# Kernel optimization log

Hardware: AMD Instinct MI355X
Metric: run time of the kernel (lower is better)

## Reference

```python
import jax, jax.numpy as jnp
import numpy as np
import math

B, S_IMG, S_TXT = 1, 2048, 256
D_MODEL, HEADS, HEAD_DIM = 3072, 24, 128
INNER = HEADS * HEAD_DIM
EPS = 1e-6


def _rmsnorm(x, scale):
    # flax-style RMSNorm over last dim, fp32 stats
    x32 = x.astype(jnp.float32)
    var = jnp.mean(x32 * x32, axis=-1, keepdims=True)
    return ((x32 * jax.lax.rsqrt(var + EPS)).astype(x.dtype)) * scale


def _rope(x, cos, sin):
    # x: [B,S,H,D]; cos,sin: [S,D]; interleaved-pair rotation (use_real_unbind_dim=-1)
    c = cos[None, :, None, :].astype(jnp.float32)
    s = sin[None, :, None, :].astype(jnp.float32)
    xp = x.reshape(*x.shape[:-1], -1, 2)
    x_rot = jnp.stack([-xp[..., 1], xp[..., 0]], axis=-1).reshape(x.shape)
    return (x.astype(jnp.float32) * c + x_rot.astype(jnp.float32) * s).astype(x.dtype)


def setup_inputs() -> dict:
    key = jax.random.key(0)
    ks = jax.random.split(key, 16)
    w = lambda k, shp: jax.random.normal(k, shp, jnp.float32) * 0.02
    S = S_TXT + S_IMG
    pos = jnp.arange(S, dtype=jnp.float32)
    inv_freq = 1.0 / (10000.0 ** (jnp.arange(0, HEAD_DIM, 2, dtype=jnp.float32) / HEAD_DIM))
    ang = pos[:, None] * inv_freq[None, :]  # [S, D/2]
    cos = jnp.repeat(jnp.cos(ang), 2, axis=-1)  # [S, D] paired layout
    sin = jnp.repeat(jnp.sin(ang), 2, axis=-1)
    return {
        'hidden_states': jax.random.normal(ks[0], (B, S_IMG, D_MODEL), jnp.float32),
        'encoder_hidden_states': jax.random.normal(ks[1], (B, S_TXT, D_MODEL), jnp.float32),
        'cos': cos,
        'sin': sin,
        'wq': w(ks[2], (D_MODEL, INNER)),
        'wk': w(ks[3], (D_MODEL, INNER)),
        'wv': w(ks[4], (D_MODEL, INNER)),
        'wq_add': w(ks[5], (D_MODEL, INNER)),
        'wk_add': w(ks[6], (D_MODEL, INNER)),
        'wv_add': w(ks[7], (D_MODEL, INNER)),
        'bq_add': w(ks[8], (INNER,)),
        'bk_add': w(ks[9], (INNER,)),
        'bv_add': w(ks[10], (INNER,)),
        'norm_q': jnp.ones((HEAD_DIM,), jnp.float32),
        'norm_k': jnp.ones((HEAD_DIM,), jnp.float32),
        'norm_add_q': jnp.ones((HEAD_DIM,), jnp.float32),
        'norm_add_k': jnp.ones((HEAD_DIM,), jnp.float32),
        'w_out': w(ks[11], (INNER, D_MODEL)),
        'b_out': w(ks[12], (D_MODEL,)),
        'w_add_out': w(ks[13], (INNER, D_MODEL)),
        'b_add_out': w(ks[14], (D_MODEL,)),
    }


def reference(hidden_states, encoder_hidden_states, cos, sin, wq, wk, wv,
              wq_add, wk_add, wv_add, bq_add, bk_add, bv_add,
              norm_q, norm_k, norm_add_q, norm_add_k,
              w_out, b_out, w_add_out, b_add_out):
    St = encoder_hidden_states.shape[1]
    heads = lambda x: x.reshape(x.shape[0], x.shape[1], HEADS, HEAD_DIM)
    # image-token q/k/v + QK RMSNorm
    q = _rmsnorm(heads(hidden_states @ wq), norm_q)
    k = _rmsnorm(heads(hidden_states @ wk), norm_k)
    v = heads(hidden_states @ wv)
    # encoder-token q/k/v (biased projections) + QK RMSNorm
    eq = _rmsnorm(heads(encoder_hidden_states @ wq_add + bq_add), norm_add_q)
    ek = _rmsnorm(heads(encoder_hidden_states @ wk_add + bk_add), norm_add_k)
    ev = heads(encoder_hidden_states @ wv_add + bv_add)
    # encoder tokens concatenated first
    q = jnp.concatenate([eq, q], axis=1)
    k = jnp.concatenate([ek, k], axis=1)
    v = jnp.concatenate([ev, v], axis=1)
    q = _rope(q, cos, sin)
    k = _rope(k, cos, sin)
    # naive softmax attention
    scale = 1.0 / math.sqrt(HEAD_DIM)
    attn = jnp.einsum('bshd,bthd->bhst', q, k) * scale
    attn = jax.nn.softmax(attn, axis=-1)
    out = jnp.einsum('bhst,bthd->bshd', attn, v)
    out = out.reshape(out.shape[0], out.shape[1], -1)
    # split back into encoder / image streams and apply output projections
    enc_out = out[:, :St] @ w_add_out + b_add_out
    img_out = out[:, St:] @ w_out + b_out
    return (img_out, enc_out)
```

## Files before the change

### kernel.cpp

```cpp
#include <hip/hip_runtime.h>
#include <hip/hip_bf16.h>

typedef unsigned short u16;
typedef unsigned int   u32;
typedef __bf16 bf16x8 __attribute__((ext_vector_type(8)));
typedef float  f32x4  __attribute__((ext_vector_type(4)));

#define SEQ   2304
#define DM    3072
#define NH    24
#define HD    128
#define S_TXT 256
#define S_IMG 2048
#define SCALE 0.08838834764831845f

__device__ __forceinline__ u16 f2bf(float x) {
  u32 u = __float_as_uint(x);
  u += 0x7fffu + ((u >> 16) & 1u);
  return (u16)(u >> 16);
}
__device__ __forceinline__ float bf2f(u16 b) {
  return __uint_as_float(((u32)b) << 16);
}
__device__ __forceinline__ f32x4 zero4() { f32x4 z = {0.f, 0.f, 0.f, 0.f}; return z; }
__device__ __forceinline__ u32 cvtpk(float lo, float hi) {
  u32 r;
  asm("v_cvt_pk_bf16_f32 %0, %1, %2" : "=v"(r) : "v"(lo), "v"(hi));
  return r;
}

#define GLDS16(gp, lp) __builtin_amdgcn_global_load_lds( \
    (__attribute__((address_space(1))) void*)(gp),       \
    (__attribute__((address_space(3))) void*)(lp), 16, 0, 0)

__global__ __launch_bounds__(256) void conv_bf16_k(const float* __restrict__ src,
                                                   u16* __restrict__ dst, int n4) {
  int i = blockIdx.x * 256 + threadIdx.x;
  if (i >= n4) return;
  float4 v = ((const float4*)src)[i];
  ushort4 o;
  o.x = f2bf(v.x); o.y = f2bf(v.y); o.z = f2bf(v.z); o.w = f2bf(v.w);
  ((ushort4*)dst)[i] = o;
}

struct WP { const float* s[8]; u16* d[8]; };

__global__ __launch_bounds__(256) void w_transpose_k(WP p) {
  __shared__ float tile[32][33];
  const float* __restrict__ src = p.s[blockIdx.z];
  u16* __restrict__ dst = p.d[blockIdx.z];
  const int c0 = blockIdx.x * 32, r0 = blockIdx.y * 32;
  const int tx = threadIdx.x & 31, ty = threadIdx.x >> 5;
#pragma unroll
  for (int i = 0; i < 4; ++i)
    tile[ty + i*8][tx] = src[(size_t)(r0 + ty + i*8) * DM + c0 + tx];
  __syncthreads();
#pragma unroll
  for (int i = 0; i < 4; ++i)
    dst[(size_t)(c0 + ty + i*8) * DM + r0 + tx] = f2bf(tile[tx][ty + i*8]);
}

__global__ __launch_bounds__(256) void v_transpose_k(const u16* __restrict__ V,
                                                     u16* __restrict__ Vt) {
  __shared__ u16 tile[32][34];
  const int h = blockIdx.z;
  const int t0 = blockIdx.x * 32, d0 = blockIdx.y * 32;
  const int tx = threadIdx.x & 31, ty = threadIdx.x >> 5;
#pragma unroll
  for (int i = 0; i < 4; ++i)
    tile[ty + i*8][tx] = V[((size_t)h * SEQ + t0 + ty + i*8) * HD + d0 + tx];
  __syncthreads();
#pragma unroll
  for (int i = 0; i < 4; ++i)
    Vt[((size_t)h * HD + d0 + ty + i*8) * SEQ + t0 + tx] = tile[tx][ty + i*8];
}

__global__ __launch_bounds__(256) void gemm_bt_k(
    const u16* __restrict__ A,
    const u16* __restrict__ B0, const u16* __restrict__ B1, const u16* __restrict__ B2,
    const float* __restrict__ bias0, const float* __restrict__ bias1, const float* __restrict__ bias2,
    void* __restrict__ out0, void* __restrict__ out1, void* __restrict__ out2,
    int row_off, int mode) {
  __shared__ __attribute__((aligned(128))) char As[128*128];
  __shared__ __attribute__((aligned(128))) char Bs[128*128];
  const int bz = blockIdx.z;
  const u16* __restrict__ Bm = (bz == 0) ? B0 : ((bz == 1) ? B1 : B2);
  const float* __restrict__ bias = (bz == 0) ? bias0 : ((bz == 1) ? bias1 : bias2);
  void* out = (bz == 0) ? out0 : ((bz == 1) ? out1 : out2);
  const int bm = blockIdx.x, bn = blockIdx.y;
  const int tid = threadIdx.x;
  const int w = tid >> 6, l = tid & 63;
  const int wr = w >> 1, wc = w & 1;

  f32x4 acc[4][4];
#pragma unroll
  for (int mi = 0; mi < 4; ++mi)
#pragma unroll
    for (int ni = 0; ni < 4; ++ni) acc[mi][ni] = zero4();

  const int srow  = l >> 3;
  const int scolb = ((l & 7) ^ srow) << 4;
  const char* Ag = (const char*)(A  + (size_t)(bm*128 + w*32) * DM) + (size_t)srow * (DM*2) + scolb;
  const char* Bg = (const char*)(Bm + (size_t)(bn*128 + w*32) * DM) + (size_t)srow * (DM*2) + scolb;
  char* AsW = As + (w*32) * 128;
  char* BsW = Bs + (w*32) * 128;

  for (int kt = 0; kt < DM/64; ++kt) {
#pragma unroll
    for (int i = 0; i < 4; ++i) {
      GLDS16(Ag + (size_t)i*8*(DM*2) + kt*128, AsW + i*8*128);
      GLDS16(Bg + (size_t)i*8*(DM*2) + kt*128, BsW + i*8*128);
    }
    __syncthreads();
#pragma unroll
    for (int kk = 0; kk < 2; ++kk) {
      bf16x8 af[4], bfr[4];
#pragma unroll
      for (int mi = 0; mi < 4; ++mi) {
        const int row = wr*64 + mi*16 + (l & 15);
        const int cb  = ((kk << 6) + ((l >> 4) << 4)) ^ ((row & 7) << 4);
        af[mi] = *(const bf16x8*)(As + row*128 + cb);
      }
#pragma unroll
      for (int ni = 0; ni < 4; ++ni) {
        const int row = wc*64 + ni*16 + (l & 15);
        const int cb  = ((kk << 6) + ((l >> 4) << 4)) ^ ((row & 7) << 4);
        bfr[ni] = *(const bf16x8*)(Bs + row*128 + cb);
      }
#pragma unroll
      for (int mi = 0; mi < 4; ++mi)
#pragma unroll
        for (int ni = 0; ni < 4; ++ni)
          acc[mi][ni] = __builtin_amdgcn_mfma_f32_16x16x32_bf16(af[mi], bfr[ni], acc[mi][ni], 0, 0, 0);
    }
    __syncthreads();
  }

#pragma unroll
  for (int mi = 0; mi < 4; ++mi) {
    const int mbase = bm*128 + wr*64 + mi*16 + ((l >> 4) << 2);
#pragma unroll
    for (int ni = 0; ni < 4; ++ni) {
      const int ncol = bn*128 + wc*64 + ni*16 + (l & 15);
      const float bv = bias ? bias[ncol] : 0.f;
#pragma unroll
      for (int r = 0; r < 4; ++r) {
        const float v = acc[mi][ni][r] + bv;
        if (mode == 0) {
          ((u16*)out)[((size_t)bn * SEQ + (row_off + mbase + r)) * HD + (ncol & 127)] = f2bf(v);
        } else {
          ((float*)out)[(size_t)(mbase + r) * DM + ncol] = v;
        }
      }
    }
  }
}

__global__ __launch_bounds__(256) void qk_norm_rope_k(
    const u16* __restrict__ Qf, const u16* __restrict__ Kf,
    u16* __restrict__ Qb, u16* __restrict__ Kb,
    const float* __restrict__ cosT, const float* __restrict__ sinT,
    const float* __restrict__ nq, const float* __restrict__ nk,
    const float* __restrict__ naq, const float* __restrict__ nak) {
  const int gw = (blockIdx.x * 256 + threadIdx.x) >> 6;
  const int l = threadIdx.x & 63;
  const int which = (gw >= NH * SEQ) ? 1 : 0;
  const int rem = which ? (gw - NH * SEQ) : gw;
  const int h = rem / SEQ, t = rem % SEQ;
  const size_t base = ((size_t)h * SEQ + t) * HD + l * 2;
  const ushort2 xb = *(const ushort2*)((which ? Kf : Qf) + base);
  const float x0 = bf2f(xb.x), x1 = bf2f(xb.y);
  float ss = x0*x0 + x1*x1;
#pragma unroll
  for (int msk = 1; msk < 64; msk <<= 1) ss += __shfl_xor(ss, msk, 64);
  const float rr = rsqrtf(ss * (1.0f/128.0f) + 1e-6f);
  const float* nw = which ? (t < S_TXT ? nak : nk) : (t < S_TXT ? naq : nq);
  const float n0 = x0 * rr * nw[l*2], n1 = x1 * rr * nw[l*2 + 1];
  const float c = cosT[(size_t)t * HD + l*2], sn = sinT[(size_t)t * HD + l*2];
  float o0 = n0 * c - n1 * sn;
  float o1 = n1 * c + n0 * sn;
  if (!which) { o0 *= SCALE; o1 *= SCALE; }
  ushort2 ob; ob.x = f2bf(o0); ob.y = f2bf(o1);
  *(ushort2*)((which ? Kb : Qb) + base) = ob;
}

__global__ __launch_bounds__(256) void attn_k(
    const u16* __restrict__ Q, const u16* __restrict__ K,
    const u16* __restrict__ Vt, u16* __restrict__ O) {
  __shared__ __attribute__((aligned(128))) char Kl[64*256];
  __shared__ __attribute__((aligned(128))) char Vl[128*128];
  __shared__ __attribute__((aligned(128))) char Pl[4][2][2048];
  const int qb = blockIdx.x, h = blockIdx.y;
  const int tid = threadIdx.x, w = tid >> 6, l = tid & 63;
  const int g = l >> 4, q16 = l & 15;

  const u16* Qh = Q  + ((size_t)h * SEQ + qb*128 + w*32) * HD;
  const u16* Kh = K  + (size_t)h * SEQ * HD;
  const u16* Vh = Vt + (size_t)h * HD * SEQ;

  bf16x8 qf[2][4];
#pragma unroll
  for (int qt = 0; qt < 2; ++qt)
#pragma unroll
    for (int kf = 0; kf < 4; ++kf)
      qf[qt][kf] = *(const bf16x8*)(Qh + (qt*16 + q16) * HD + kf*32 + g*8);

  f32x4 o[2][8];
#pragma unroll
  for (int qt = 0; qt < 2; ++qt)
#pragma unroll
    for (int db = 0; db < 8; ++db) o[qt][db] = zero4();
  float m[2]  = {-3e38f, -3e38f};
  float rl[2] = {0.f, 0.f};

  const int vswz = ((l & 7) ^ (l >> 3)) << 4;
  const int pswz = (q16 & 7) << 4;

  for (int kb = 0; kb < SEQ/64; ++kb) {
#pragma unroll
    for (int i = 0; i < 4; ++i) {
      const int rloc = i*4 + (l >> 4);
      const int colb = ((l & 15) << 4) ^ ((rloc & 7) << 4);
      GLDS16((const char*)Kh + ((size_t)(kb*64 + w*16 + rloc)) * 256 + colb,
             Kl + (w*16 + i*4) * 256);
    }
#pragma unroll
    for (int i = 0; i < 4; ++i) {
      const int rloc = w*32 + i*8 + (l >> 3);
      GLDS16((const char*)Vh + (size_t)rloc * (SEQ*2) + kb*128 + vswz,
             Vl + (w*32 + i*8) * 128);
    }
    __syncthreads();

    f32x4 s[2][4];
#pragma unroll
    for (int qt = 0; qt < 2; ++qt)
#pragma unroll
      for (int mi = 0; mi < 4; ++mi) s[qt][mi] = zero4();
#pragma unroll
    for (int mi = 0; mi < 4; ++mi) {
      const int row = mi*16 + q16;
      bf16x8 kfr[4];
#pragma unroll
      for (int kf = 0; kf < 4; ++kf) {
        const int cb = ((kf << 6) + (g << 4)) ^ ((row & 7) << 4);
        kfr[kf] = *(const bf16x8*)(Kl + row*256 + cb);
      }
#pragma unroll
      for (int kf = 0; kf < 4; ++kf) {
        s[0][mi] = __builtin_amdgcn_mfma_f32_16x16x32_bf16(kfr[kf], qf[0][kf], s[0][mi], 0, 0, 0);
        s[1][mi] = __builtin_amdgcn_mfma_f32_16x16x32_bf16(kfr[kf], qf[1][kf], s[1][mi], 0, 0, 0);
      }
    }

    float rsv[2];
#pragma unroll
    for (int qt = 0; qt < 2; ++qt) {
      float mx = s[qt][0][0];
#pragma unroll
      for (int mi = 0; mi < 4; ++mi)
#pragma unroll
        for (int r = 0; r < 4; ++r) mx = fmaxf(mx, s[qt][mi][r]);
      mx = fmaxf(mx, __shfl_xor(mx, 16, 64));
      mx = fmaxf(mx, __shfl_xor(mx, 32, 64));
      const float mn = fmaxf(m[qt], mx);
      rsv[qt] = __expf(m[qt] - mn);
      m[qt] = mn;
      float sum = 0.f;
#pragma unroll
      for (int mi = 0; mi < 4; ++mi) {
        f32x4 t = s[qt][mi];
#pragma unroll
        for (int r = 0; r < 4; ++r) { t[r] = __expf(t[r] - mn); sum += t[r]; }
        s[qt][mi] = t;
      }
      sum += __shfl_xor(sum, 16, 64);
      sum += __shfl_xor(sum, 32, 64);
      rl[qt] = rl[qt] * rsv[qt] + sum;
      char* Pw = Pl[w][qt];
#pragma unroll
      for (int mi = 0; mi < 4; ++mi) {
        uint2 pk;
        pk.x = cvtpk(s[qt][mi][0], s[qt][mi][1]);
        pk.y = cvtpk(s[qt][mi][2], s[qt][mi][3]);
        *(uint2*)(Pw + ((q16*128 + mi*32 + g*8) ^ pswz)) = pk;
      }
    }

#pragma unroll
    for (int qt = 0; qt < 2; ++qt) {
      float rs4[4];
#pragma unroll
      for (int r = 0; r < 4; ++r)
        rs4[r] = __shfl(rsv[qt], (g << 4) + (g << 2) + r, 64);
#pragma unroll
      for (int db = 0; db < 8; ++db) {
        f32x4 t = o[qt][db];
#pragma unroll
        for (int r = 0; r < 4; ++r) t[r] *= rs4[r];
        o[qt][db] = t;
      }
    }

    bf16x8 pa[2][2];
#pragma unroll
    for (int qt = 0; qt < 2; ++qt)
#pragma unroll
      for (int kblk = 0; kblk < 2; ++kblk)
        pa[qt][kblk] = *(const bf16x8*)(Pl[w][qt] + ((q16*128 + kblk*64 + g*16) ^ pswz));

#pragma unroll
    for (int kblk = 0; kblk < 2; ++kblk)
#pragma unroll
      for (int db = 0; db < 8; ++db) {
        const int vrow = db*16 + q16;
        const int vcb  = ((kblk << 6) + (g << 4)) ^ ((vrow & 7) << 4);
        bf16x8 vb = *(const bf16x8*)(Vl + vrow*128 + vcb);
        o[0][db] = __builtin_amdgcn_mfma_f32_16x16x32_bf16(pa[0][kblk], vb, o[0][db], 0, 0, 0);
        o[1][db] = __builtin_amdgcn_mfma_f32_16x16x32_bf16(pa[1][kblk], vb, o[1][db], 0, 0, 0);
      }
    __syncthreads();
  }

#pragma unroll
  for (int qt = 0; qt < 2; ++qt) {
    float inv4[4];
#pragma unroll
    for (int r = 0; r < 4; ++r)
      inv4[r] = 1.f / __shfl(rl[qt], (g << 4) + (g << 2) + r, 64);
#pragma unroll
    for (int db = 0; db < 8; ++db)
#pragma unroll
      for (int r = 0; r < 4; ++r) {
        const int token = qb*128 + w*32 + qt*16 + g*4 + r;
        const int col = h*HD + db*16 + q16;
        O[(size_t)token * DM + col] = f2bf(o[qt][db][r] * inv4[r]);
      }
  }
}

extern "C" void kernel_launch(void* const* d_in, const int* in_sizes, int n_in,
                              void* d_out, int out_size, void* d_ws, size_t ws_size,
                              hipStream_t stream) {
  const float* hidden = (const float*)d_in[0];
  const float* ench   = (const float*)d_in[1];
  const float* cosT   = (const float*)d_in[2];
  const float* sinT   = (const float*)d_in[3];
  const float* wq  = (const float*)d_in[4];
  const float* wk  = (const float*)d_in[5];
  const float* wv  = (const float*)d_in[6];
  const float* wqa = (const float*)d_in[7];
  const float* wka = (const float*)d_in[8];
  const float* wva = (const float*)d_in[9];
  const float* bqa = (const float*)d_in[10];
  const float* bka = (const float*)d_in[11];
  const float* bva = (const float*)d_in[12];
  const float* nq  = (const float*)d_in[13];
  const float* nk  = (const float*)d_in[14];
  const float* naq = (const float*)d_in[15];
  const float* nak = (const float*)d_in[16];
  const float* w_out     = (const float*)d_in[17];
  const float* b_out     = (const float*)d_in[18];
  const float* w_add_out = (const float*)d_in[19];
  const float* b_add_out = (const float*)d_in[20];
  float* outp = (float*)d_out;
  (void)in_sizes; (void)n_in; (void)out_size; (void)ws_size;

  char* ws = (char*)d_ws;
  size_t off = 0;
  auto alloc = [&](size_t n) { char* p = ws + off; off += (n + 255) & ~(size_t)255; return p; };
  u16* wt[8];
  for (int i = 0; i < 8; ++i) wt[i] = (u16*)alloc((size_t)DM * DM * 2);
  u16* xb_img = (u16*)alloc((size_t)S_IMG * DM * 2);
  u16* xb_enc = (u16*)alloc((size_t)S_TXT * DM * 2);
  u16* Qf = (u16*)alloc((size_t)NH * SEQ * HD * 2);
  u16* Kf = (u16*)alloc((size_t)NH * SEQ * HD * 2);
  u16* Vf = (u16*)alloc((size_t)NH * SEQ * HD * 2);
  u16* Qb = (u16*)alloc((size_t)NH * SEQ * HD * 2);
  u16* Kb = (u16*)alloc((size_t)NH * SEQ * HD * 2);
  u16* Vt = (u16*)alloc((size_t)NH * HD * SEQ * 2);
  u16* Ob = (u16*)alloc((size_t)SEQ * DM * 2);

  conv_bf16_k<<<(S_IMG*DM/4)/256, 256, 0, stream>>>(hidden, xb_img, S_IMG*DM/4);
  conv_bf16_k<<<(S_TXT*DM/4)/256, 256, 0, stream>>>(ench, xb_enc, S_TXT*DM/4);

  WP wp;
  wp.s[0] = wq;  wp.s[1] = wk;  wp.s[2] = wv;
  wp.s[3] = wqa; wp.s[4] = wka; wp.s[5] = wva;
  wp.s[6] = w_out; wp.s[7] = w_add_out;
  for (int i = 0; i < 8; ++i) wp.d[i] = wt[i];
  w_transpose_k<<<dim3(96, 96, 8), 256, 0, stream>>>(wp);

  gemm_bt_k<<<dim3(16, 24, 3), 256, 0, stream>>>(xb_img, wt[0], wt[1], wt[2],
      nullptr, nullptr, nullptr, Qf, Kf, Vf, S_TXT, 0);
  gemm_bt_k<<<dim3(2, 24, 3), 256, 0, stream>>>(xb_enc, wt[3], wt[4], wt[5],
      bqa, bka, bva, Qf, Kf, Vf, 0, 0);

  qk_norm_rope_k<<<(2*NH*SEQ)/4, 256, 0, stream>>>(Qf, Kf, Qb, Kb, cosT, sinT, nq, nk, naq, nak);
  v_transpose_k<<<dim3(SEQ/32, HD/32, NH), 256, 0, stream>>>(Vf, Vt);

  attn_k<<<dim3(SEQ/128, NH), 256, 0, stream>>>(Qb, Kb, Vt, Ob);

  gemm_bt_k<<<dim3(16, 24, 1), 256, 0, stream>>>(Ob + (size_t)S_TXT * DM, wt[6], wt[6], wt[6],
      b_out, b_out, b_out, outp, outp, outp, 0, 1);
  gemm_bt_k<<<dim3(2, 24, 1), 256, 0, stream>>>(Ob, wt[7], wt[7], wt[7],
      b_add_out, b_add_out, b_add_out,
      outp + (size_t)S_IMG * DM, outp + (size_t)S_IMG * DM, outp + (size_t)S_IMG * DM, 0, 1);
}
```

Measured before the change: 937.8 us.

## Double-buffer attention K/V tiles, remap attention blocks, merge enc/img GEMM launches

The attention kernel now double-buffers its K and V shared-memory tiles, prefetching the next tile while computing the current one. It replaces __syncthreads with explicit waitcnt and barrier calls and raises wave priority around the MFMA sections. The attention grid is flattened and remapped so blocks are spread across XCDs by head. The separate encoder and image QKV and output-projection GEMMs are merged into single launches over a concatenated activation buffer, choosing weights and bias per row block. This removes kernel launches and tail effects, at the cost of more LDS use per attention block, which may reduce occupancy.

```diff
diff --git a/kernel.cpp b/kernel.cpp
--- a/kernel.cpp
+++ b/kernel.cpp
@@ -75,19 +75,28 @@
     Vt[((size_t)h * HD + d0 + ty + i*8) * SEQ + t0 + tx] = tile[tx][ty + i*8];
 }
 
-__global__ __launch_bounds__(256) void gemm_bt_k(
-    const u16* __restrict__ A,
-    const u16* __restrict__ B0, const u16* __restrict__ B1, const u16* __restrict__ B2,
-    const float* __restrict__ bias0, const float* __restrict__ bias1, const float* __restrict__ bias2,
-    void* __restrict__ out0, void* __restrict__ out1, void* __restrict__ out2,
-    int row_off, int mode) {
+struct GArgs {
+  const u16* A;
+  const u16* Bimg0; const u16* Bimg1; const u16* Bimg2;
+  const u16* Benc0; const u16* Benc1; const u16* Benc2;
+  const float* bEnc0; const float* bEnc1; const float* bEnc2;
+  const float* bImg;
+  void* out0; void* out1; void* out2;
+  int mode;
+};
+
+__global__ __launch_bounds__(256) void gemm_bt_k(GArgs p) {
   __shared__ __attribute__((aligned(128))) char As[128*128];
   __shared__ __attribute__((aligned(128))) char Bs[128*128];
   const int bz = blockIdx.z;
-  const u16* __restrict__ Bm = (bz == 0) ? B0 : ((bz == 1) ? B1 : B2);
-  const float* __restrict__ bias = (bz == 0) ? bias0 : ((bz == 1) ? bias1 : bias2);
-  void* out = (bz == 0) ? out0 : ((bz == 1) ? out1 : out2);
   const int bm = blockIdx.x, bn = blockIdx.y;
+  const bool enc = (bm < 2);
+  const u16* __restrict__ Bm = (bz == 0) ? (enc ? p.Benc0 : p.Bimg0)
+                             : (bz == 1) ? (enc ? p.Benc1 : p.Bimg1)
+                                         : (enc ? p.Benc2 : p.Bimg2);
+  const float* __restrict__ bias = enc ? ((bz == 0) ? p.bEnc0 : (bz == 1) ? p.bEnc1 : p.bEnc2)
+                                       : p.bImg;
+  void* out = (bz == 0) ? p.out0 : (bz == 1) ? p.out1 : p.out2;
   const int tid = threadIdx.x;
   const int w = tid >> 6, l = tid & 63;
   const int wr = w >> 1, wc = w & 1;
@@ -100,8 +109,8 @@
 
   const int srow  = l >> 3;
   const int scolb = ((l & 7) ^ srow) << 4;
-  const char* Ag = (const char*)(A  + (size_t)(bm*128 + w*32) * DM) + (size_t)srow * (DM*2) + scolb;
-  const char* Bg = (const char*)(Bm + (size_t)(bn*128 + w*32) * DM) + (size_t)srow * (DM*2) + scolb;
+  const char* Ag = (const char*)(p.A + (size_t)(bm*128 + w*32) * DM) + (size_t)srow * (DM*2) + scolb;
+  const char* Bg = (const char*)(Bm  + (size_t)(bn*128 + w*32) * DM) + (size_t)srow * (DM*2) + scolb;
   char* AsW = As + (w*32) * 128;
   char* BsW = Bs + (w*32) * 128;
 
@@ -146,10 +155,12 @@
 #pragma unroll
       for (int r = 0; r < 4; ++r) {
         const float v = acc[mi][ni][r] + bv;
-        if (mode == 0) {
-          ((u16*)out)[((size_t)bn * SEQ + (row_off + mbase + r)) * HD + (ncol & 127)] = f2bf(v);
+        const int row = mbase + r;
+        if (p.mode == 0) {
+          ((u16*)out)[((size_t)bn * SEQ + row) * HD + (ncol & 127)] = f2bf(v);
         } else {
-          ((float*)out)[(size_t)(mbase + r) * DM + ncol] = v;
+          const size_t orow = (row < S_TXT) ? (size_t)(S_IMG + row) : (size_t)(row - S_TXT);
+          ((float*)out)[orow * DM + ncol] = v;
         }
       }
     }
@@ -187,12 +198,15 @@
 __global__ __launch_bounds__(256) void attn_k(
     const u16* __restrict__ Q, const u16* __restrict__ K,
     const u16* __restrict__ Vt, u16* __restrict__ O) {
-  __shared__ __attribute__((aligned(128))) char Kl[64*256];
-  __shared__ __attribute__((aligned(128))) char Vl[128*128];
-  __shared__ __attribute__((aligned(128))) char Pl[4][2][2048];
-  const int qb = blockIdx.x, h = blockIdx.y;
+  __shared__ __attribute__((aligned(128))) char Kl[2][64*256];
+  __shared__ __attribute__((aligned(128))) char Vl[2][128*128];
+  __shared__ __attribute__((aligned(128))) char Pl[4][2048];
+  const int orig = blockIdx.x;
+  const int lin = (orig & 7) * 54 + (orig >> 3);
+  const int h = lin / 18, qb = lin % 18;
   const int tid = threadIdx.x, w = tid >> 6, l = tid & 63;
   const int g = l >> 4, q16 = l & 15;
+  const int NT = SEQ / 64;
 
   const u16* Qh = Q  + ((size_t)h * SEQ + qb*128 + w*32) * HD;
   const u16* Kh = K  + (size_t)h * SEQ * HD;
@@ -216,27 +230,44 @@
   const int vswz = ((l & 7) ^ (l >> 3)) << 4;
   const int pswz = (q16 & 7) << 4;
 
-  for (int kb = 0; kb < SEQ/64; ++kb) {
+  auto STAGE = [&](int buf, int kb) {
 #pragma unroll
     for (int i = 0; i < 4; ++i) {
       const int rloc = i*4 + (l >> 4);
       const int colb = ((l & 15) << 4) ^ ((rloc & 7) << 4);
       GLDS16((const char*)Kh + ((size_t)(kb*64 + w*16 + rloc)) * 256 + colb,
-             Kl + (w*16 + i*4) * 256);
+             &Kl[buf][(w*16 + i*4) * 256]);
     }
 #pragma unroll
     for (int i = 0; i < 4; ++i) {
       const int rloc = w*32 + i*8 + (l >> 3);
       GLDS16((const char*)Vh + (size_t)rloc * (SEQ*2) + kb*128 + vswz,
-             Vl + (w*32 + i*8) * 128);
-    }
-    __syncthreads();
+             &Vl[buf][(w*32 + i*8) * 128]);
+    }
+  };
+
+  STAGE(0, 0);
+  int cur = 0;
+
+  for (int kb = 0; kb < NT; ++kb) {
+    if (kb + 1 < NT) {
+      STAGE(cur ^ 1, kb + 1);
+      asm volatile("s_waitcnt vmcnt(8)" ::: "memory");
+    } else {
+      asm volatile("s_waitcnt vmcnt(0)" ::: "memory");
+    }
+    __builtin_amdgcn_s_barrier();
+    __builtin_amdgcn_sched_barrier(0);
+
+    const char* Kb_ = Kl[cur];
+    const char* Vb_ = Vl[cur];
 
     f32x4 s[2][4];
 #pragma unroll
     for (int qt = 0; qt < 2; ++qt)
 #pragma unroll
       for (int mi = 0; mi < 4; ++mi) s[qt][mi] = zero4();
+    __builtin_amdgcn_s_setprio(1);
 #pragma unroll
     for (int mi = 0; mi < 4; ++mi) {
       const int row = mi*16 + q16;
@@ -244,7 +275,7 @@
 #pragma unroll
       for (int kf = 0; kf < 4; ++kf) {
         const int cb = ((kf << 6) + (g << 4)) ^ ((row & 7) << 4);
-        kfr[kf] = *(const bf16x8*)(Kl + row*256 + cb);
+        kfr[kf] = *(const bf16x8*)(Kb_ + row*256 + cb);
       }
 #pragma unroll
       for (int kf = 0; kf < 4; ++kf) {
@@ -252,8 +283,11 @@
         s[1][mi] = __builtin_amdgcn_mfma_f32_16x16x32_bf16(kfr[kf], qf[1][kf], s[1][mi], 0, 0, 0);
       }
     }
+    __builtin_amdgcn_s_setprio(0);
 
     float rsv[2];
+    bf16x8 pa[2][2];
+    char* Pw = Pl[w];
 #pragma unroll
     for (int qt = 0; qt < 2; ++qt) {
       float mx = s[qt][0][0];
@@ -277,7 +311,6 @@
       sum += __shfl_xor(sum, 16, 64);
       sum += __shfl_xor(sum, 32, 64);
       rl[qt] = rl[qt] * rsv[qt] + sum;
-      char* Pw = Pl[w][qt];
 #pragma unroll
       for (int mi = 0; mi < 4; ++mi) {
         uint2 pk;
@@ -285,6 +318,9 @@
         pk.y = cvtpk(s[qt][mi][2], s[qt][mi][3]);
         *(uint2*)(Pw + ((q16*128 + mi*32 + g*8) ^ pswz)) = pk;
       }
+#pragma unroll
+      for (int kblk = 0; kblk < 2; ++kblk)
+        pa[qt][kblk] = *(const bf16x8*)(Pw + ((q16*128 + kblk*64 + g*16) ^ pswz));
     }
 
 #pragma unroll
@@ -302,24 +338,23 @@
       }
     }
 
-    bf16x8 pa[2][2];
-#pragma unroll
-    for (int qt = 0; qt < 2; ++qt)
-#pragma unroll
-      for (int kblk = 0; kblk < 2; ++kblk)
-        pa[qt][kblk] = *(const bf16x8*)(Pl[w][qt] + ((q16*128 + kblk*64 + g*16) ^ pswz));
-
+    __builtin_amdgcn_s_setprio(1);
 #pragma unroll
     for (int kblk = 0; kblk < 2; ++kblk)
 #pragma unroll
       for (int db = 0; db < 8; ++db) {
         const int vrow = db*16 + q16;
         const int vcb  = ((kblk << 6) + (g << 4)) ^ ((vrow & 7) << 4);
-        bf16x8 vb = *(const bf16x8*)(Vl + vrow*128 + vcb);
+        bf16x8 vb = *(const bf16x8*)(Vb_ + vrow*128 + vcb);
         o[0][db] = __builtin_amdgcn_mfma_f32_16x16x32_bf16(pa[0][kblk], vb, o[0][db], 0, 0, 0);
         o[1][db] = __builtin_amdgcn_mfma_f32_16x16x32_bf16(pa[1][kblk], vb, o[1][db], 0, 0, 0);
       }
-    __syncthreads();
+    __builtin_amdgcn_s_setprio(0);
+
+    asm volatile("s_waitcnt lgkmcnt(0)" ::: "memory");
+    __builtin_amdgcn_s_barrier();
+    __builtin_amdgcn_sched_barrier(0);
+    cur ^= 1;
   }
 
 #pragma unroll
@@ -371,8 +406,7 @@
   auto alloc = [&](size_t n) { char* p = ws + off; off += (n + 255) & ~(size_t)255; return p; };
   u16* wt[8];
   for (int i = 0; i < 8; ++i) wt[i] = (u16*)alloc((size_t)DM * DM * 2);
-  u16* xb_img = (u16*)alloc((size_t)S_IMG * DM * 2);
-  u16* xb_enc = (u16*)alloc((size_t)S_TXT * DM * 2);
+  u16* xb = (u16*)alloc((size_t)SEQ * DM * 2);
   u16* Qf = (u16*)alloc((size_t)NH * SEQ * HD * 2);
   u16* Kf = (u16*)alloc((size_t)NH * SEQ * HD * 2);
   u16* Vf = (u16*)alloc((size_t)NH * SEQ * HD * 2);
@@ -381,8 +415,8 @@
   u16* Vt = (u16*)alloc((size_t)NH * HD * SEQ * 2);
   u16* Ob = (u16*)alloc((size_t)SEQ * DM * 2);
 
-  conv_bf16_k<<<(S_IMG*DM/4)/256, 256, 0, stream>>>(hidden, xb_img, S_IMG*DM/4);
-  conv_bf16_k<<<(S_TXT*DM/4)/256, 256, 0, stream>>>(ench, xb_enc, S_TXT*DM/4);
+  conv_bf16_k<<<(S_TXT*DM/4)/256, 256, 0, stream>>>(ench, xb, S_TXT*DM/4);
+  conv_bf16_k<<<(S_IMG*DM/4)/256, 256, 0, stream>>>(hidden, xb + (size_t)S_TXT*DM, S_IMG*DM/4);
 
   WP wp;
   wp.s[0] = wq;  wp.s[1] = wk;  wp.s[2] = wv;
@@ -391,19 +425,28 @@
   for (int i = 0; i < 8; ++i) wp.d[i] = wt[i];
   w_transpose_k<<<dim3(96, 96, 8), 256, 0, stream>>>(wp);
 
-  gemm_bt_k<<<dim3(16, 24, 3), 256, 0, stream>>>(xb_img, wt[0], wt[1], wt[2],
-      nullptr, nullptr, nullptr, Qf, Kf, Vf, S_TXT, 0);
-  gemm_bt_k<<<dim3(2, 24, 3), 256, 0, stream>>>(xb_enc, wt[3], wt[4], wt[5],
-      bqa, bka, bva, Qf, Kf, Vf, 0, 0);
+  GArgs qkv;
+  qkv.A = xb;
+  qkv.Bimg0 = wt[0]; qkv.Bimg1 = wt[1]; qkv.Bimg2 = wt[2];
+  qkv.Benc0 = wt[3]; qkv.Benc1 = wt[4]; qkv.Benc2 = wt[5];
+  qkv.bEnc0 = bqa;   qkv.bEnc1 = bka;   qkv.bEnc2 = bva;
+  qkv.bImg  = nullptr;
+  qkv.out0 = Qf; qkv.out1 = Kf; qkv.out2 = Vf;
+  qkv.mode = 0;
+  gemm_bt_k<<<dim3(18, 24, 3), 256, 0, stream>>>(qkv);
 
   qk_norm_rope_k<<<(2*NH*SEQ)/4, 256, 0, stream>>>(Qf, Kf, Qb, Kb, cosT, sinT, nq, nk, naq, nak);
   v_transpose_k<<<dim3(SEQ/32, HD/32, NH), 256, 0, stream>>>(Vf, Vt);
 
-  attn_k<<<dim3(SEQ/128, NH), 256, 0, stream>>>(Qb, Kb, Vt, Ob);
-
-  gemm_bt_k<<<dim3(16, 24, 1), 256, 0, stream>>>(Ob + (size_t)S_TXT * DM, wt[6], wt[6], wt[6],
-      b_out, b_out, b_out, outp, outp, outp, 0, 1);
-  gemm_bt_k<<<dim3(2, 24, 1), 256, 0, stream>>>(Ob, wt[7], wt[7], wt[7],
-      b_add_out, b_add_out, b_add_out,
-      outp + (size_t)S_IMG * DM, outp + (size_t)S_IMG * DM, outp + (size_t)S_IMG * DM, 0, 1);
-}
+  attn_k<<<432, 256, 0, stream>>>(Qb, Kb, Vt, Ob);
+
+  GArgs op;
+  op.A = Ob;
+  op.Bimg0 = wt[6]; op.Bimg1 = wt[6]; op.Bimg2 = wt[6];
+  op.Benc0 = wt[7]; op.Benc1 = wt[7]; op.Benc2 = wt[7];
+  op.bEnc0 = b_add_out; op.bEnc1 = b_add_out; op.bEnc2 = b_add_out;
+  op.bImg  = b_out;
+  op.out0 = outp; op.out1 = outp; op.out2 = outp;
+  op.mode = 1;
+  gemm_bt_k<<<dim3(18, 24, 1), 256, 0, stream>>>(op);
+}
```

After: 781.0 us. 16.7% less time.
